# Kernel optimization log

Measured on AMD Instinct MI355X. Metric: run time of the kernel, lower is better.

Reference implementation:

```python
import jax, jax.numpy as jnp
import numpy as np

EMB = 1024
HEADS = 8
SEQ = 4096
LN_EPS = 1e-5


def _layernorm(x, g, b):
    mu = jnp.mean(x, axis=-1, keepdims=True)
    var = jnp.mean(jnp.square(x - mu), axis=-1, keepdims=True)
    return (x - mu) * jax.lax.rsqrt(var + LN_EPS) * g + b


def setup_inputs() -> dict:
    key = jax.random.key(0)
    ks = jax.random.split(key, 12)
    s = 1.0 / np.sqrt(EMB)
    sz = 1.0 / np.sqrt(EMB * HEADS)
    return {
        "history": jax.random.normal(ks[0], (SEQ, EMB), jnp.float32),
        "embdding": jax.random.normal(ks[1], (SEQ, EMB), jnp.float32),
        # per-head Linear weights, torch layout [out, in], stacked over heads
        "Wq_w": jax.random.uniform(ks[2], (HEADS, EMB, EMB), jnp.float32, -s, s),
        "Wq_b": jax.random.uniform(ks[3], (HEADS, EMB), jnp.float32, -s, s),
        "Wk_w": jax.random.uniform(ks[4], (HEADS, EMB, EMB), jnp.float32, -s, s),
        "Wk_b": jax.random.uniform(ks[5], (HEADS, EMB), jnp.float32, -s, s),
        "Wv_w": jax.random.uniform(ks[6], (HEADS, EMB, EMB), jnp.float32, -s, s),
        "Wv_b": jax.random.uniform(ks[7], (HEADS, EMB), jnp.float32, -s, s),
        "Wz_w": jax.random.uniform(ks[8], (EMB, EMB * HEADS), jnp.float32, -sz, sz),
        "Wz_b": jax.random.uniform(ks[9], (EMB,), jnp.float32, -sz, sz),
        "ln1_g": jnp.ones((EMB,), jnp.float32),
        "ln1_b": jnp.zeros((EMB,), jnp.float32),
        "Wf_w": jax.random.uniform(ks[10], (EMB, EMB), jnp.float32, -s, s),
        "Wf_b": jax.random.uniform(ks[11], (EMB,), jnp.float32, -s, s),
        "ln2_g": jnp.ones((EMB,), jnp.float32),
        "ln2_b": jnp.zeros((EMB,), jnp.float32),
    }


def reference(history, embdding, Wq_w, Wq_b, Wk_w, Wk_b, Wv_w, Wv_b,
              Wz_w, Wz_b, ln1_g, ln1_b, Wf_w, Wf_b, ln2_g, ln2_b):
    S, E = embdding.shape
    H = Wq_w.shape[0]
    # per-head linears (torch: y = x @ W.T + b), batched over heads
    Q = jnp.einsum('se,hfe->hsf', embdding, Wq_w) + Wq_b[:, None, :]  # [H,S,E]
    K = jnp.einsum('se,hfe->hsf', embdding, Wk_w) + Wk_b[:, None, :]
    V = jnp.einsum('se,hfe->hsf', history, Wv_w) + Wv_b[:, None, :]
    # K^T @ Q -> [H, E, E], softmax over dim=1 of the 2D matrix == last axis here
    scores = jnp.einsum('hse,hsf->hef', K, Q) / jnp.sqrt(jnp.asarray(E, Q.dtype))
    A = jax.nn.softmax(scores, axis=-1)  # [H,E,E]
    Zh = jnp.einsum('hse,hef->hsf', V, A)  # [H,S,E]
    Z = jnp.transpose(Zh, (1, 0, 2)).reshape(S, H * E)  # cat(dim=1) in head order
    O = Z @ Wz_w.T + Wz_b  # [S,E]
    LN1 = _layernorm(O, ln1_g, ln1_b) + embdding
    FN = LN1 @ Wf_w.T + Wf_b
    LN2 = _layernorm(FN, ln2_g, ln2_b) + LN1
    return LN2
```

## Files before the change

### kernel.cpp

```cpp
#include <hip/hip_runtime.h>


constexpr int EMB = 1024;
constexpr int SEQ = 4096;
constexpr int NH  = 8;

using f32x4  = __attribute__((ext_vector_type(4))) float;
using bf16x8 = __attribute__((ext_vector_type(8))) __bf16;
using us8    = __attribute__((ext_vector_type(8))) unsigned short;

#define GLOAD_LDS16(g, l) __builtin_amdgcn_global_load_lds(                 \
    (const __attribute__((address_space(1))) void*)(g),                     \
    (__attribute__((address_space(3))) void*)(l), 16, 0, 0)

__device__ inline unsigned short f2bf(float x) {
  unsigned int u = __float_as_uint(x);
  u += 0x7FFFu + ((u >> 16) & 1u);
  return (unsigned short)(u >> 16);
}
__device__ inline float bf2f(unsigned short h) {
  return __uint_as_float(((unsigned int)h) << 16);
}

constexpr int NB_DOTB = 4096;
constexpr int NB_ROWB = 1664;
constexpr int NB_XT   = 1024;

__global__ __launch_bounds__(256) void mega_cvt_k(
    const float* __restrict__ Wk, const float* __restrict__ Wq,
    const float* __restrict__ hist, const float* __restrict__ Wz,
    const float* __restrict__ Wf, const float* __restrict__ emb,
    const float* __restrict__ Wv, const float* __restrict__ xbar,
    unsigned short* __restrict__ Wkb, unsigned short* __restrict__ Wqb,
    unsigned short* __restrict__ Yb, unsigned short* __restrict__ Wzb,
    unsigned short* __restrict__ Wfb, unsigned short* __restrict__ XT,
    unsigned short* __restrict__ WvT,
    float* __restrict__ u, float* __restrict__ v) {
  __shared__ float tileT[64][65];
  const int b = blockIdx.x, tid = threadIdx.x;

  if (b < NB_DOTB) {
    int gw = b * 4 + (tid >> 6);
    int lane = tid & 63;
    const float* src = (gw < 8192) ? Wk : Wq;
    unsigned short* dst = (gw < 8192) ? Wkb : Wqb;
    float* dot = (gw < 8192) ? u : v;
    int row = gw & 8191;
    const float4* sr = (const float4*)(src + (size_t)row * EMB);
    const float4* xb4 = (const float4*)xbar;
    ushort4* d4 = (ushort4*)(dst + (size_t)row * EMB);
    float s = 0.f;
#pragma unroll
    for (int j = 0; j < 4; ++j) {
      int idx = j * 64 + lane;
      float4 x = sr[idx];
      float4 xb = xb4[idx];
      ushort4 o; o.x = f2bf(x.x); o.y = f2bf(x.y); o.z = f2bf(x.z); o.w = f2bf(x.w);
      d4[idx] = o;
      s += x.x * xb.x + x.y * xb.y + x.z * xb.z + x.w * xb.w;
    }
#pragma unroll
    for (int off = 32; off; off >>= 1) s += __shfl_down(s, off);
    if (lane == 0) dot[row] = s;
  } else if (b < NB_DOTB + NB_ROWB) {
    size_t f0 = (size_t)(b - NB_DOTB) * 8192;
    const float* src; unsigned short* dst; size_t loc;
    if (f0 < 4194304ull) { src = hist; dst = Yb; loc = f0; }
    else if (f0 < 12582912ull) { src = Wz; dst = Wzb; loc = f0 - 4194304ull; }
    else { src = Wf; dst = Wfb; loc = f0 - 12582912ull; }
#pragma unroll
    for (int p = 0; p < 8; ++p) {
      int i = p * 256 + tid;
      float4 x = ((const float4*)(src + loc))[i];
      ushort4 o; o.x = f2bf(x.x); o.y = f2bf(x.y); o.z = f2bf(x.z); o.w = f2bf(x.w);
      ((ushort4*)(dst + loc))[i] = o;
    }
  } else {
    int tb = b - (NB_DOTB + NB_ROWB);
    const float* src; unsigned short* dst; int R, r0, c0;
    if (tb < NB_XT) {
      src = emb; dst = XT; R = SEQ;
      r0 = (tb >> 4) * 64; c0 = (tb & 15) * 64;
    } else {
      int t2 = tb - NB_XT, z = t2 >> 8, tt = t2 & 255;
      src = Wv + (size_t)z * EMB * EMB; dst = WvT + (size_t)z * EMB * EMB;
      R = EMB;
      r0 = (tt >> 4) * 64; c0 = (tt & 15) * 64;
    }
    int tx = tid & 15, ty = tid >> 4;
#pragma unroll
    for (int p = 0; p < 4; ++p) {
      int ir = p * 16 + ty;
      float4 x = *(const float4*)(src + (size_t)(r0 + ir) * EMB + c0 + tx * 4);
      tileT[tx * 4 + 0][ir] = x.x; tileT[tx * 4 + 1][ir] = x.y;
      tileT[tx * 4 + 2][ir] = x.z; tileT[tx * 4 + 3][ir] = x.w;
    }
    __syncthreads();
#pragma unroll
    for (int p = 0; p < 4; ++p) {
      int orow = p * 16 + ty;
      ushort4 o;
      o.x = f2bf(tileT[orow][tx * 4 + 0]);
      o.y = f2bf(tileT[orow][tx * 4 + 1]);
      o.z = f2bf(tileT[orow][tx * 4 + 2]);
      o.w = f2bf(tileT[orow][tx * 4 + 3]);
      *(ushort4*)(dst + (size_t)(c0 + orow) * R + r0 + tx * 4) = o;
    }
  }
}

__global__ __launch_bounds__(256) void colsum_part_k(const float* __restrict__ X,
                                                     float* __restrict__ part) {
  int e = blockIdx.x * 256 + threadIdx.x;
  int y = blockIdx.y;
  float s = 0.f;
  for (int r = y * 128; r < y * 128 + 128; ++r) s += X[(size_t)r * EMB + e];
  part[y * EMB + e] = s;
}
__global__ __launch_bounds__(256) void colsum_red_k(const float* __restrict__ part,
                                                    float* __restrict__ xbar) {
  int e = blockIdx.x * 256 + threadIdx.x;
  float s = 0.f;
  for (int y = 0; y < 32; ++y) s += part[y * EMB + e];
  xbar[e] = s;
}

__global__ __launch_bounds__(256) void dvec_k(const unsigned short* __restrict__ Wzb,
                                              const float* __restrict__ bz,
                                              const float* __restrict__ c,
                                              float* __restrict__ d) {
  __shared__ float sb[4];
  int g = blockIdx.x, tid = threadIdx.x;
  const unsigned short* row = Wzb + (size_t)g * (NH * EMB);
  float s = 0.f;
#pragma unroll
  for (int p = 0; p < 4; ++p) {
    int i = p * 256 + tid;
    us8 w = ((const us8*)row)[i];
    float4 c0 = ((const float4*)c)[i * 2];
    float4 c1 = ((const float4*)c)[i * 2 + 1];
    s += bf2f(w[0]) * c0.x + bf2f(w[1]) * c0.y + bf2f(w[2]) * c0.z + bf2f(w[3]) * c0.w;
    s += bf2f(w[4]) * c1.x + bf2f(w[5]) * c1.y + bf2f(w[6]) * c1.z + bf2f(w[7]) * c1.w;
  }
  int lane = tid & 63, w = tid >> 6;
#pragma unroll
  for (int off = 32; off; off >>= 1) s += __shfl_down(s, off);
  if (lane == 0) sb[w] = s;
  __syncthreads();
  if (tid == 0) d[g] = bz[g] + sb[0] + sb[1] + sb[2] + sb[3];
}

__global__ __launch_bounds__(256) void mred_tr_k(const unsigned short* __restrict__ Mp,
                                                 unsigned short* __restrict__ MT) {
  __shared__ float t[32][33];
  int g0 = blockIdx.x * 32, e0 = blockIdx.y * 32;
  int tx = threadIdx.x & 31, ty = threadIdx.x >> 5;
#pragma unroll
  for (int k = 0; k < 4; ++k) {
    int e = e0 + ty + k * 8;
    float s = 0.f;
#pragma unroll
    for (int h = 0; h < NH; ++h)
      s += bf2f(Mp[((size_t)h << 20) + (size_t)e * EMB + g0 + tx]);
    t[ty + k * 8][tx] = s;
  }
  __syncthreads();
#pragma unroll
  for (int k = 0; k < 4; ++k) {
    int r = ty + k * 8;
    MT[(size_t)(g0 + r) * EMB + e0 + tx] = f2bf(t[tx][r]);
  }
}

__global__ __launch_bounds__(256) void gram_red_k(const unsigned short* __restrict__ Gp,
                                                  unsigned short* __restrict__ Gbf) {
  int i = blockIdx.x * 256 + threadIdx.x;
  float4 s = {0.f, 0.f, 0.f, 0.f};
#pragma unroll
  for (int z = 0; z < 8; ++z) {
    ushort4 v = ((const ushort4*)(Gp + (size_t)z * EMB * EMB))[i];
    s.x += bf2f(v.x); s.y += bf2f(v.y); s.z += bf2f(v.z); s.w += bf2f(v.w);
  }
  ushort4 o; o.x = f2bf(s.x); o.y = f2bf(s.y); o.z = f2bf(s.z); o.w = f2bf(s.w);
  ((ushort4*)Gbf)[i] = o;
}

__global__ __launch_bounds__(256) void colstat1_k(const unsigned short* __restrict__ ScT,
                                                  float* __restrict__ m_part,
                                                  float* __restrict__ s_part) {
  int col = blockIdx.x * 256 + threadIdx.x;
  int rc = blockIdx.y, h = blockIdx.z;
  const unsigned short* base = ScT + ((size_t)h * EMB + rc * 64) * EMB + col;
  float m = -1e30f, s = 0.f;
#pragma unroll 4
  for (int r = 0; r < 64; ++r) {
    float x = bf2f(base[(size_t)r * EMB]);
    float nm = fmaxf(m, x);
    s = s * __expf(m - nm) + __expf(x - nm);
    m = nm;
  }
  m_part[((size_t)h * 16 + rc) * EMB + col] = m;
  s_part[((size_t)h * 16 + rc) * EMB + col] = s;
}

__global__ __launch_bounds__(256) void colstat2_k(const float* __restrict__ m_part,
                                                  const float* __restrict__ s_part,
                                                  float* __restrict__ mfin,
                                                  float* __restrict__ isfin) {
  int i = blockIdx.x * 256 + threadIdx.x;
  int h = i >> 10, col = i & 1023;
  float M = -1e30f, S = 0.f;
#pragma unroll
  for (int c = 0; c < 16; ++c) {
    float m = m_part[((size_t)h * 16 + c) * EMB + col];
    float s = s_part[((size_t)h * 16 + c) * EMB + col];
    float nm = fmaxf(M, m);
    S = S * __expf(M - nm) + s * __expf(m - nm);
    M = nm;
  }
  mfin[i] = M;
  isfin[i] = 1.0f / S;
}

__global__ __launch_bounds__(256) void at_cvec_k(const unsigned short* __restrict__ ScT,
                                                 const float* __restrict__ mfin,
                                                 const float* __restrict__ isfin,
                                                 const float* __restrict__ bv,
                                                 unsigned short* __restrict__ AT,
                                                 float* __restrict__ cbuf) {
  __shared__ float sb[4];
  int f = blockIdx.x, h = blockIdx.y, tid = threadIdx.x;
  size_t rowoff = ((size_t)h * EMB + f) * EMB;
  ushort4 xr = ((const ushort4*)(ScT + rowoff))[tid];
  float4 m  = ((const float4*)(mfin + (size_t)h * EMB))[tid];
  float4 is = ((const float4*)(isfin + (size_t)h * EMB))[tid];
  float4 b  = ((const float4*)(bv + (size_t)h * EMB))[tid];
  float a0 = __expf(bf2f(xr.x) - m.x) * is.x;
  float a1 = __expf(bf2f(xr.y) - m.y) * is.y;
  float a2 = __expf(bf2f(xr.z) - m.z) * is.z;
  float a3 = __expf(bf2f(xr.w) - m.w) * is.w;
  ushort4 o; o.x = f2bf(a0); o.y = f2bf(a1); o.z = f2bf(a2); o.w = f2bf(a3);
  ((ushort4*)(AT + rowoff))[tid] = o;
  float s = a0 * b.x + a1 * b.y + a2 * b.z + a3 * b.w;
  int lane = tid & 63, w = tid >> 6;
#pragma unroll
  for (int off = 32; off; off >>= 1) s += __shfl_down(s, off);
  if (lane == 0) sb[w] = s;
  __syncthreads();
  if (tid == 0) cbuf[h * EMB + f] = sb[0] + sb[1] + sb[2] + sb[3];
}

__global__ __launch_bounds__(256) void layernorm_k(const float* __restrict__ Xin,
                                                   const float* __restrict__ resid,
                                                   const float* __restrict__ gw,
                                                   const float* __restrict__ bw,
                                                   float* __restrict__ outf,
                                                   unsigned short* __restrict__ outb) {
  __shared__ float sb[16];
  int row = blockIdx.x, tid = threadIdx.x;
  float4 v = ((const float4*)(Xin + (size_t)row * EMB))[tid];
  float s = v.x + v.y + v.z + v.w;
  float q = v.x * v.x + v.y * v.y + v.z * v.z + v.w * v.w;
  int lane = tid & 63, w = tid >> 6;
#pragma unroll
  for (int off = 32; off; off >>= 1) { s += __shfl_down(s, off); q += __shfl_down(q, off); }
  if (lane == 0) { sb[w] = s; sb[8 + w] = q; }
  __syncthreads();
  float mu  = (sb[0] + sb[1] + sb[2] + sb[3]) * (1.0f / EMB);
  float var = (sb[8] + sb[9] + sb[10] + sb[11]) * (1.0f / EMB) - mu * mu;
  float rs = rsqrtf(var + 1e-5f);
  float4 rv = ((const float4*)(resid + (size_t)row * EMB))[tid];
  float4 gv = ((const float4*)gw)[tid];
  float4 bv = ((const float4*)bw)[tid];
  float o0 = (v.x - mu) * rs * gv.x + bv.x + rv.x;
  float o1 = (v.y - mu) * rs * gv.y + bv.y + rv.y;
  float o2 = (v.z - mu) * rs * gv.z + bv.z + rv.z;
  float o3 = (v.w - mu) * rs * gv.w + bv.w + rv.w;
  float4 ov; ov.x = o0; ov.y = o1; ov.z = o2; ov.w = o3;
  ((float4*)(outf + (size_t)row * EMB))[tid] = ov;
  if (outb) {
    ushort4 ob; ob.x = f2bf(o0); ob.y = f2bf(o1); ob.z = f2bf(o2); ob.w = f2bf(o3);
    ((ushort4*)(outb + (size_t)row * EMB))[tid] = ob;
  }
}

template <int MODE>
__global__ __launch_bounds__(256) void gemm_nt(const unsigned short* __restrict__ A,
                                               const unsigned short* __restrict__ B,
                                               void* __restrict__ Cout,
                                               int K, int lda, int ldb, int ldc,
                                               long long aZ, long long bZ, long long cZ,
                                               int nx, int ny,
                                               const float* __restrict__ e0,
                                               const float* __restrict__ e1,
                                               const float* __restrict__ e2,
                                               const float* __restrict__ e3) {
  const int q = gridDim.x >> 3;
  const int wg = (blockIdx.x & 7) * q + (blockIdx.x >> 3);
  const int bx = wg % nx;
  const int by = (wg / nx) % ny;
  const int z  = wg / (nx * ny);
  A += (size_t)z * aZ;
  B += (size_t)z * bZ;
  const int tid = threadIdx.x;
  const int lane = tid & 63, wid = tid >> 6;
  const int wm = wid >> 1, wn = wid & 1;
  const int row0 = bx * 64, col0 = by * 128;

  __shared__ __align__(16) unsigned short lds[(64 + 128) * 64];
  unsigned short* As = lds;
  unsigned short* Bs = lds + 64 * 64;

  f32x4 acc[2][4] = {};
  const int lrow = lane & 15, kg = lane >> 4;
  const int lr = lane >> 3;
  const int lc = (lane & 7) * 8;

  const int nt = K >> 6;
  for (int t = 0; t < nt; ++t) {
    const int k0 = t << 6;
#pragma unroll
    for (int c = 0; c < 2; ++c) {
      int chunk = wid * 2 + c;
      int r = chunk * 8 + lr;
      GLOAD_LDS16(A + (size_t)(row0 + r) * lda + k0 + lc, &As[chunk * 512]);
    }
#pragma unroll
    for (int c = 0; c < 4; ++c) {
      int chunk = wid * 4 + c;
      int r = chunk * 8 + lr;
      GLOAD_LDS16(B + (size_t)(col0 + r) * ldb + k0 + lc, &Bs[chunk * 512]);
    }
    __syncthreads();
#pragma unroll
    for (int ks = 0; ks < 2; ++ks) {
      bf16x8 a[2], b[4];
      int koff = ks * 32 + kg * 8;
#pragma unroll
      for (int i = 0; i < 2; ++i)
        a[i] = *(const bf16x8*)&As[(wm * 32 + i * 16 + lrow) * 64 + koff];
#pragma unroll
      for (int j = 0; j < 4; ++j)
        b[j] = *(const bf16x8*)&Bs[(wn * 64 + j * 16 + lrow) * 64 + koff];
#pragma unroll
      for (int i = 0; i < 2; ++i)
#pragma unroll
        for (int j = 0; j < 4; ++j)
          acc[i][j] = __builtin_amdgcn_mfma_f32_16x16x32_bf16(a[i], b[j], acc[i][j], 0, 0, 0);
    }
    __syncthreads();
  }

  const int rb = (lane >> 4) * 4, cc = lane & 15;
  if (MODE == 1 || MODE == 4) {
    unsigned short* Cs = lds;
#pragma unroll
    for (int i = 0; i < 2; ++i) {
#pragma unroll
      for (int j = 0; j < 4; ++j) {
#pragma unroll
        for (int r = 0; r < 4; ++r) {
          float val = acc[i][j][r];
          int mm = wm * 32 + i * 16 + rb + r;
          int nn = wn * 64 + j * 16 + cc;
          if (MODE == 4) {
            int m = row0 + mm, n = col0 + nn;
            float bq = e0[z * EMB + m], uu = e1[z * EMB + n];
            float bk = e2[z * EMB + n], vv = e3[z * EMB + m];
            val = (val + bq * (uu + (float)SEQ * bk) + vv * bk) * (1.0f / 32.0f);
          }
          Cs[mm * 128 + nn] = f2bf(val);
        }
      }
    }
    __syncthreads();
    unsigned short* Cg = (unsigned short*)Cout + (size_t)z * cZ;
#pragma unroll
    for (int p = 0; p < 4; ++p) {
      int idx = p * 256 + tid;
      int row = idx >> 4, col = (idx & 15) * 8;
      *(us8*)(Cg + (size_t)(row0 + row) * ldc + col0 + col) =
          *(const us8*)&Cs[row * 128 + col];
    }
  } else {
#pragma unroll
    for (int i = 0; i < 2; ++i) {
#pragma unroll
      for (int j = 0; j < 4; ++j) {
#pragma unroll
        for (int r = 0; r < 4; ++r) {
          int m = row0 + wm * 32 + i * 16 + rb + r;
          int n = col0 + wn * 64 + j * 16 + cc;
          size_t off = (size_t)z * cZ + (size_t)m * ldc + n;
          ((float*)Cout)[off] = acc[i][j][r] + e0[n];
        }
      }
    }
  }
}

extern "C" void kernel_launch(void* const* d_in, const int* in_sizes, int n_in,
                              void* d_out, int out_size, void* d_ws, size_t ws_size,
                              hipStream_t stream) {
  const float* history = (const float*)d_in[0];
  const float* emb     = (const float*)d_in[1];
  const float* Wq_w = (const float*)d_in[2];
  const float* Wq_b = (const float*)d_in[3];
  const float* Wk_w = (const float*)d_in[4];
  const float* Wk_b = (const float*)d_in[5];
  const float* Wv_w = (const float*)d_in[6];
  const float* Wv_b = (const float*)d_in[7];
  const float* Wz_w = (const float*)d_in[8];
  const float* Wz_b = (const float*)d_in[9];
  const float* ln1_g = (const float*)d_in[10];
  const float* ln1_b = (const float*)d_in[11];
  const float* Wf_w = (const float*)d_in[12];
  const float* Wf_b = (const float*)d_in[13];
  const float* ln2_g = (const float*)d_in[14];
  const float* ln2_b = (const float*)d_in[15];

  char* ws = (char*)d_ws;
  const size_t MB = 1024ull * 1024ull;
  unsigned short* XT  = (unsigned short*)(ws + 0);
  unsigned short* Ybf = (unsigned short*)(ws + 8 * MB);
  unsigned short* Wkb = (unsigned short*)(ws + 16 * MB);
  unsigned short* Wqb = (unsigned short*)(ws + 32 * MB);
  unsigned short* WvT = (unsigned short*)(ws + 48 * MB);
  unsigned short* Wzb = (unsigned short*)(ws + 64 * MB);
  unsigned short* Wfb = (unsigned short*)(ws + 80 * MB);
  unsigned short* Gbf = (unsigned short*)(ws + 82 * MB);
  float* xpart = (float*)(ws + 84 * MB);
  float* xbar  = (float*)(ws + 84 * MB + 160 * 1024);
  float* ubuf  = (float*)(ws + 84 * MB + 192 * 1024);
  float* vbuf  = (float*)(ws + 84 * MB + 256 * 1024);
  float* cbuf  = (float*)(ws + 84 * MB + 320 * 1024);
  float* dbuf  = (float*)(ws + 84 * MB + 384 * 1024);
  unsigned short* Tbf = (unsigned short*)(ws + 85 * MB);
  float* Sc  = (float*)(ws + 101 * MB);
  char*  St  = ws + 133 * MB;
  unsigned short* ATb = (unsigned short*)(ws + 149 * MB);
  unsigned short* MTb = (unsigned short*)(ws + 165 * MB);
  float* m_part = (float*)(St);
  float* s_part = (float*)(St + 512 * 1024);
  float* mfin   = (float*)(St + 1024 * 1024);
  float* isfin  = (float*)(St + 1056 * 1024);
  unsigned short* Gp  = (unsigned short*)Sc;
  unsigned short* ScT = (unsigned short*)Sc;
  unsigned short* Cbf = Tbf;
  unsigned short* Mp  = (unsigned short*)Sc;
  float* Obuf = (float*)St;
  float* LN1  = (float*)ATb;
  unsigned short* LN1b = XT;
  float* FN   = (float*)Tbf;
  const long long EE = (long long)EMB * EMB;

  colsum_part_k<<<dim3(4, 32), 256, 0, stream>>>(emb, xpart);
  colsum_red_k<<<dim3(4), 256, 0, stream>>>(xpart, xbar);

  mega_cvt_k<<<dim3(8832), 256, 0, stream>>>(Wk_w, Wq_w, history, Wz_w, Wf_w,
                                             emb, Wv_w, xbar,
                                             Wkb, Wqb, Ybf, Wzb, Wfb, XT, WvT,
                                             ubuf, vbuf);

  gemm_nt<1><<<dim3(1024), 256, 0, stream>>>(XT, XT, Gp, 512, SEQ, SEQ, EMB,
                                             512, 512, EE, 16, 8,
                                             nullptr, nullptr, nullptr, nullptr);
  gram_red_k<<<dim3(EMB * EMB / 4 / 256), 256, 0, stream>>>(Gp, Gbf);
  gemm_nt<1><<<dim3(1024), 256, 0, stream>>>(Wqb, Gbf, Tbf, EMB, EMB, EMB, EMB,
                                             EE, 0, EE, 16, 8,
                                             nullptr, nullptr, nullptr, nullptr);
  gemm_nt<4><<<dim3(1024), 256, 0, stream>>>(Tbf, Wkb, ScT, EMB, EMB, EMB, EMB,
                                             EE, EE, EE, 16, 8,
                                             Wq_b, ubuf, Wk_b, vbuf);
  colstat1_k<<<dim3(4, 16, NH), 256, 0, stream>>>(ScT, m_part, s_part);
  colstat2_k<<<dim3(32), 256, 0, stream>>>(m_part, s_part, mfin, isfin);
  at_cvec_k<<<dim3(EMB, NH), 256, 0, stream>>>(ScT, mfin, isfin, Wv_b, ATb, cbuf);
  gemm_nt<1><<<dim3(1024), 256, 0, stream>>>(WvT, ATb, Cbf, EMB, EMB, EMB, EMB,
                                             EE, EE, EE, 16, 8,
                                             nullptr, nullptr, nullptr, nullptr);
  gemm_nt<1><<<dim3(1024), 256, 0, stream>>>(Cbf, Wzb, Mp, EMB, EMB, NH * EMB, EMB,
                                             EE, (long long)EMB, EE, 16, 8,
                                             nullptr, nullptr, nullptr, nullptr);
  mred_tr_k<<<dim3(EMB / 32, EMB / 32), 256, 0, stream>>>(Mp, MTb);
  dvec_k<<<dim3(EMB), 256, 0, stream>>>(Wzb, Wz_b, cbuf, dbuf);
  gemm_nt<3><<<dim3(512), 256, 0, stream>>>(Ybf, MTb, Obuf, EMB, EMB, EMB, EMB,
                                            0, 0, 0, 64, 8,
                                            dbuf, nullptr, nullptr, nullptr);
  layernorm_k<<<dim3(SEQ), 256, 0, stream>>>(Obuf, emb, ln1_g, ln1_b, LN1, LN1b);
  gemm_nt<3><<<dim3(512), 256, 0, stream>>>(LN1b, Wfb, FN, EMB, EMB, EMB, EMB,
                                            0, 0, 0, 64, 8,
                                            Wf_b, nullptr, nullptr, nullptr);
  layernorm_k<<<dim3(SEQ), 256, 0, stream>>>(FN, LN1, ln2_g, ln2_b, (float*)d_out, nullptr);
}
```

Before: 292.6 us.

## Co-schedule independent kernels: fold Gram GEMM into conversion kernel and dvec into Mp GEMM

Moves the emb transpose/bf16 conversion into the column-sum kernel, then launches the Gram GEMM in the same grid as the weight conversions so the two independent jobs run concurrently. The dvec reduction likewise shares a launch with the Mp GEMM. The GEMM body becomes a shared device function. This removes launches and tail idle time, at the cost of heterogeneous blocks competing for memory bandwidth and LDS.

```diff
diff --git a/kernel.cpp b/kernel.cpp
--- a/kernel.cpp
+++ b/kernel.cpp
@@ -22,31 +22,204 @@
   return __uint_as_float(((unsigned int)h) << 16);
 }
 
-constexpr int NB_DOTB = 4096;
-constexpr int NB_ROWB = 1664;
-constexpr int NB_XT   = 1024;
-
-__global__ __launch_bounds__(256) void mega_cvt_k(
+template <int MODE>
+__device__ __attribute__((always_inline)) void gemm_body(
+    unsigned short* lds, int wg,
+    const unsigned short* A, const unsigned short* B, void* Cout,
+    int K, int lda, int ldb, int ldc,
+    long long aZ, long long bZ, long long cZ, int nx, int ny,
+    const float* e0, const float* e1, const float* e2, const float* e3) {
+  const int bx = wg % nx;
+  const int by = (wg / nx) % ny;
+  const int z  = wg / (nx * ny);
+  A += (size_t)z * aZ;
+  B += (size_t)z * bZ;
+  const int tid = threadIdx.x;
+  const int lane = tid & 63, wid = tid >> 6;
+  const int wm = wid >> 1, wn = wid & 1;
+  const int row0 = bx * 64, col0 = by * 128;
+
+  unsigned short* As = lds;
+  unsigned short* Bs = lds + 64 * 64;
+
+  f32x4 acc[2][4] = {};
+  const int lrow = lane & 15, kg = lane >> 4;
+  const int lr = lane >> 3;
+  const int lc = (lane & 7) * 8;
+
+  const int nt = K >> 6;
+  for (int t = 0; t < nt; ++t) {
+    const int k0 = t << 6;
+#pragma unroll
+    for (int c = 0; c < 2; ++c) {
+      int chunk = wid * 2 + c;
+      int r = chunk * 8 + lr;
+      GLOAD_LDS16(A + (size_t)(row0 + r) * lda + k0 + lc, &As[chunk * 512]);
+    }
+#pragma unroll
+    for (int c = 0; c < 4; ++c) {
+      int chunk = wid * 4 + c;
+      int r = chunk * 8 + lr;
+      GLOAD_LDS16(B + (size_t)(col0 + r) * ldb + k0 + lc, &Bs[chunk * 512]);
+    }
+    __syncthreads();
+#pragma unroll
+    for (int ks = 0; ks < 2; ++ks) {
+      bf16x8 a[2], b[4];
+      int koff = ks * 32 + kg * 8;
+#pragma unroll
+      for (int i = 0; i < 2; ++i)
+        a[i] = *(const bf16x8*)&As[(wm * 32 + i * 16 + lrow) * 64 + koff];
+#pragma unroll
+      for (int j = 0; j < 4; ++j)
+        b[j] = *(const bf16x8*)&Bs[(wn * 64 + j * 16 + lrow) * 64 + koff];
+#pragma unroll
+      for (int i = 0; i < 2; ++i)
+#pragma unroll
+        for (int j = 0; j < 4; ++j)
+          acc[i][j] = __builtin_amdgcn_mfma_f32_16x16x32_bf16(a[i], b[j], acc[i][j], 0, 0, 0);
+    }
+    __syncthreads();
+  }
+
+  const int rb = (lane >> 4) * 4, cc = lane & 15;
+  if (MODE == 1 || MODE == 4) {
+    unsigned short* Cs = lds;
+#pragma unroll
+    for (int i = 0; i < 2; ++i) {
+#pragma unroll
+      for (int j = 0; j < 4; ++j) {
+#pragma unroll
+        for (int r = 0; r < 4; ++r) {
+          float val = acc[i][j][r];
+          int mm = wm * 32 + i * 16 + rb + r;
+          int nn = wn * 64 + j * 16 + cc;
+          if (MODE == 4) {
+            int m = row0 + mm, n = col0 + nn;
+            float bq = e0[z * EMB + m], uu = e1[z * EMB + n];
+            float bk = e2[z * EMB + n], vv = e3[z * EMB + m];
+            val = (val + bq * (uu + (float)SEQ * bk) + vv * bk) * (1.0f / 32.0f);
+          }
+          Cs[mm * 128 + nn] = f2bf(val);
+        }
+      }
+    }
+    __syncthreads();
+    unsigned short* Cg = (unsigned short*)Cout + (size_t)z * cZ;
+#pragma unroll
+    for (int p = 0; p < 4; ++p) {
+      int idx = p * 256 + tid;
+      int row = idx >> 4, col = (idx & 15) * 8;
+      *(us8*)(Cg + (size_t)(row0 + row) * ldc + col0 + col) =
+          *(const us8*)&Cs[row * 128 + col];
+    }
+  } else {
+#pragma unroll
+    for (int i = 0; i < 2; ++i) {
+#pragma unroll
+      for (int j = 0; j < 4; ++j) {
+#pragma unroll
+        for (int r = 0; r < 4; ++r) {
+          int m = row0 + wm * 32 + i * 16 + rb + r;
+          int n = col0 + wn * 64 + j * 16 + cc;
+          size_t off = (size_t)z * cZ + (size_t)m * ldc + n;
+          ((float*)Cout)[off] = acc[i][j][r] + e0[n];
+        }
+      }
+    }
+  }
+}
+
+template <int MODE>
+__global__ __launch_bounds__(256) void gemm_nt(const unsigned short* __restrict__ A,
+                                               const unsigned short* __restrict__ B,
+                                               void* __restrict__ Cout,
+                                               int K, int lda, int ldb, int ldc,
+                                               long long aZ, long long bZ, long long cZ,
+                                               int nx, int ny,
+                                               const float* __restrict__ e0,
+                                               const float* __restrict__ e1,
+                                               const float* __restrict__ e2,
+                                               const float* __restrict__ e3) {
+  __shared__ __align__(16) unsigned short lds[(64 + 128) * 64];
+  const int q = gridDim.x >> 3;
+  const int wg = (blockIdx.x & 7) * q + (blockIdx.x >> 3);
+  gemm_body<MODE>(lds, wg, A, B, Cout, K, lda, ldb, ldc, aZ, bZ, cZ, nx, ny,
+                  e0, e1, e2, e3);
+}
+
+__global__ __launch_bounds__(256) void colsum_xt_k(const float* __restrict__ emb,
+                                                   float* __restrict__ part,
+                                                   unsigned short* __restrict__ XT) {
+  __shared__ float tileT[64][65];
+  const int b = blockIdx.x, tid = threadIdx.x;
+  if (b < 128) {
+    int e = (b & 3) * 256 + tid;
+    int y = b >> 2;
+    float s = 0.f;
+    for (int r = y * 128; r < y * 128 + 128; ++r) s += emb[(size_t)r * EMB + e];
+    part[y * EMB + e] = s;
+    return;
+  }
+  int tb = b - 128;
+  int r0 = (tb >> 4) * 64, c0 = (tb & 15) * 64;
+  int tx = tid & 15, ty = tid >> 4;
+#pragma unroll
+  for (int p = 0; p < 4; ++p) {
+    int ir = p * 16 + ty;
+    float4 x = *(const float4*)(emb + (size_t)(r0 + ir) * EMB + c0 + tx * 4);
+    tileT[tx * 4 + 0][ir] = x.x; tileT[tx * 4 + 1][ir] = x.y;
+    tileT[tx * 4 + 2][ir] = x.z; tileT[tx * 4 + 3][ir] = x.w;
+  }
+  __syncthreads();
+#pragma unroll
+  for (int p = 0; p < 4; ++p) {
+    int orow = p * 16 + ty;
+    ushort4 o;
+    o.x = f2bf(tileT[orow][tx * 4 + 0]);
+    o.y = f2bf(tileT[orow][tx * 4 + 1]);
+    o.z = f2bf(tileT[orow][tx * 4 + 2]);
+    o.w = f2bf(tileT[orow][tx * 4 + 3]);
+    *(ushort4*)(XT + (size_t)(c0 + orow) * SEQ + r0 + tx * 4) = o;
+  }
+}
+
+__global__ __launch_bounds__(256) void colsum_red_k(const float* __restrict__ part,
+                                                    float* __restrict__ xbar) {
+  int e = blockIdx.x * 256 + threadIdx.x;
+  float s = 0.f;
+  for (int y = 0; y < 32; ++y) s += part[y * EMB + e];
+  xbar[e] = s;
+}
+
+__global__ __launch_bounds__(256) void gram_cvt_k(
+    const unsigned short* __restrict__ XT, unsigned short* __restrict__ Gp,
     const float* __restrict__ Wk, const float* __restrict__ Wq,
     const float* __restrict__ hist, const float* __restrict__ Wz,
-    const float* __restrict__ Wf, const float* __restrict__ emb,
-    const float* __restrict__ Wv, const float* __restrict__ xbar,
+    const float* __restrict__ Wf, const float* __restrict__ Wv,
+    const float* __restrict__ xbar,
     unsigned short* __restrict__ Wkb, unsigned short* __restrict__ Wqb,
     unsigned short* __restrict__ Yb, unsigned short* __restrict__ Wzb,
-    unsigned short* __restrict__ Wfb, unsigned short* __restrict__ XT,
-    unsigned short* __restrict__ WvT,
+    unsigned short* __restrict__ Wfb, unsigned short* __restrict__ WvT,
     float* __restrict__ u, float* __restrict__ v) {
-  __shared__ float tileT[64][65];
-  const int b = blockIdx.x, tid = threadIdx.x;
-
-  if (b < NB_DOTB) {
-    int gw = b * 4 + (tid >> 6);
+  __shared__ __align__(16) unsigned short smem[(64 + 128) * 64];
+  const int tid = threadIdx.x;
+  if (blockIdx.x < 1024) {
+    const int wg = ((int)blockIdx.x & 7) * 128 + ((int)blockIdx.x >> 3);
+    gemm_body<1>(smem, wg, XT, XT, Gp, 512, SEQ, SEQ, EMB,
+                 512, 512, (long long)EMB * EMB, 16, 8,
+                 nullptr, nullptr, nullptr, nullptr);
+    return;
+  }
+  int b2 = blockIdx.x - 1024;
+  if (b2 < 4096) {
+    int gw = b2 * 4 + (tid >> 6);
     int lane = tid & 63;
     const float* src = (gw < 8192) ? Wk : Wq;
     unsigned short* dst = (gw < 8192) ? Wkb : Wqb;
     float* dot = (gw < 8192) ? u : v;
     int row = gw & 8191;
-    const float4* sr = (const float4*)(src + (size_t)row * EMB);
+    const float4* sr  = (const float4*)(src + (size_t)row * EMB);
     const float4* xb4 = (const float4*)xbar;
     ushort4* d4 = (ushort4*)(dst + (size_t)row * EMB);
     float s = 0.f;
@@ -62,8 +235,8 @@
 #pragma unroll
     for (int off = 32; off; off >>= 1) s += __shfl_down(s, off);
     if (lane == 0) dot[row] = s;
-  } else if (b < NB_DOTB + NB_ROWB) {
-    size_t f0 = (size_t)(b - NB_DOTB) * 8192;
+  } else if (b2 < 5760) {
+    size_t f0 = (size_t)(b2 - 4096) * 8192;
     const float* src; unsigned short* dst; size_t loc;
     if (f0 < 4194304ull) { src = hist; dst = Yb; loc = f0; }
     else if (f0 < 12582912ull) { src = Wz; dst = Wzb; loc = f0 - 4194304ull; }
@@ -76,17 +249,11 @@
       ((ushort4*)(dst + loc))[i] = o;
     }
   } else {
-    int tb = b - (NB_DOTB + NB_ROWB);
-    const float* src; unsigned short* dst; int R, r0, c0;
-    if (tb < NB_XT) {
-      src = emb; dst = XT; R = SEQ;
-      r0 = (tb >> 4) * 64; c0 = (tb & 15) * 64;
-    } else {
-      int t2 = tb - NB_XT, z = t2 >> 8, tt = t2 & 255;
-      src = Wv + (size_t)z * EMB * EMB; dst = WvT + (size_t)z * EMB * EMB;
-      R = EMB;
-      r0 = (tt >> 4) * 64; c0 = (tt & 15) * 64;
-    }
+    int t2 = b2 - 5760, z = t2 >> 8, tt = t2 & 255;
+    const float* src = Wv + (size_t)z * EMB * EMB;
+    unsigned short* dst = WvT + (size_t)z * EMB * EMB;
+    int r0 = (tt >> 4) * 64, c0 = (tt & 15) * 64;
+    float (*tileT)[65] = (float(*)[65])smem;
     int tx = tid & 15, ty = tid >> 4;
 #pragma unroll
     for (int p = 0; p < 4; ++p) {
@@ -104,41 +271,35 @@
       o.y = f2bf(tileT[orow][tx * 4 + 1]);
       o.z = f2bf(tileT[orow][tx * 4 + 2]);
       o.w = f2bf(tileT[orow][tx * 4 + 3]);
-      *(ushort4*)(dst + (size_t)(c0 + orow) * R + r0 + tx * 4) = o;
-    }
-  }
-}
-
-__global__ __launch_bounds__(256) void colsum_part_k(const float* __restrict__ X,
-                                                     float* __restrict__ part) {
-  int e = blockIdx.x * 256 + threadIdx.x;
-  int y = blockIdx.y;
-  float s = 0.f;
-  for (int r = y * 128; r < y * 128 + 128; ++r) s += X[(size_t)r * EMB + e];
-  part[y * EMB + e] = s;
-}
-__global__ __launch_bounds__(256) void colsum_red_k(const float* __restrict__ part,
-                                                    float* __restrict__ xbar) {
-  int e = blockIdx.x * 256 + threadIdx.x;
-  float s = 0.f;
-  for (int y = 0; y < 32; ++y) s += part[y * EMB + e];
-  xbar[e] = s;
-}
-
-__global__ __launch_bounds__(256) void dvec_k(const unsigned short* __restrict__ Wzb,
-                                              const float* __restrict__ bz,
-                                              const float* __restrict__ c,
-                                              float* __restrict__ d) {
-  __shared__ float sb[4];
-  int g = blockIdx.x, tid = threadIdx.x;
+      *(ushort4*)(dst + (size_t)(c0 + orow) * EMB + r0 + tx * 4) = o;
+    }
+  }
+}
+
+__global__ __launch_bounds__(256) void mp_dvec_k(
+    const unsigned short* __restrict__ Cbf, const unsigned short* __restrict__ Wzb,
+    unsigned short* __restrict__ Mp,
+    const float* __restrict__ bz, const float* __restrict__ cvec,
+    float* __restrict__ d) {
+  __shared__ __align__(16) unsigned short smem[(64 + 128) * 64];
+  const int tid = threadIdx.x;
+  if (blockIdx.x < 1024) {
+    const int wg = ((int)blockIdx.x & 7) * 128 + ((int)blockIdx.x >> 3);
+    gemm_body<1>(smem, wg, Cbf, Wzb, Mp, EMB, EMB, NH * EMB, EMB,
+                 (long long)EMB * EMB, (long long)EMB, (long long)EMB * EMB, 16, 8,
+                 nullptr, nullptr, nullptr, nullptr);
+    return;
+  }
+  int g = blockIdx.x - 1024;
+  float* sb = (float*)smem;
   const unsigned short* row = Wzb + (size_t)g * (NH * EMB);
   float s = 0.f;
 #pragma unroll
   for (int p = 0; p < 4; ++p) {
     int i = p * 256 + tid;
     us8 w = ((const us8*)row)[i];
-    float4 c0 = ((const float4*)c)[i * 2];
-    float4 c1 = ((const float4*)c)[i * 2 + 1];
+    float4 c0 = ((const float4*)cvec)[i * 2];
+    float4 c1 = ((const float4*)cvec)[i * 2 + 1];
     s += bf2f(w[0]) * c0.x + bf2f(w[1]) * c0.y + bf2f(w[2]) * c0.z + bf2f(w[3]) * c0.w;
     s += bf2f(w[4]) * c1.x + bf2f(w[5]) * c1.y + bf2f(w[6]) * c1.z + bf2f(w[7]) * c1.w;
   }
@@ -281,121 +442,6 @@
   if (outb) {
     ushort4 ob; ob.x = f2bf(o0); ob.y = f2bf(o1); ob.z = f2bf(o2); ob.w = f2bf(o3);
     ((ushort4*)(outb + (size_t)row * EMB))[tid] = ob;
-  }
-}
-
-template <int MODE>
-__global__ __launch_bounds__(256) void gemm_nt(const unsigned short* __restrict__ A,
-                                               const unsigned short* __restrict__ B,
-                                               void* __restrict__ Cout,
-                                               int K, int lda, int ldb, int ldc,
-                                               long long aZ, long long bZ, long long cZ,
-                                               int nx, int ny,
-                                               const float* __restrict__ e0,
-                                               const float* __restrict__ e1,
-                                               const float* __restrict__ e2,
-                                               const float* __restrict__ e3) {
-  const int q = gridDim.x >> 3;
-  const int wg = (blockIdx.x & 7) * q + (blockIdx.x >> 3);
-  const int bx = wg % nx;
-  const int by = (wg / nx) % ny;
-  const int z  = wg / (nx * ny);
-  A += (size_t)z * aZ;
-  B += (size_t)z * bZ;
-  const int tid = threadIdx.x;
-  const int lane = tid & 63, wid = tid >> 6;
-  const int wm = wid >> 1, wn = wid & 1;
-  const int row0 = bx * 64, col0 = by * 128;
-
-  __shared__ __align__(16) unsigned short lds[(64 + 128) * 64];
-  unsigned short* As = lds;
-  unsigned short* Bs = lds + 64 * 64;
-
-  f32x4 acc[2][4] = {};
-  const int lrow = lane & 15, kg = lane >> 4;
-  const int lr = lane >> 3;
-  const int lc = (lane & 7) * 8;
-
-  const int nt = K >> 6;
-  for (int t = 0; t < nt; ++t) {
-    const int k0 = t << 6;
-#pragma unroll
-    for (int c = 0; c < 2; ++c) {
-      int chunk = wid * 2 + c;
-      int r = chunk * 8 + lr;
-      GLOAD_LDS16(A + (size_t)(row0 + r) * lda + k0 + lc, &As[chunk * 512]);
-    }
-#pragma unroll
-    for (int c = 0; c < 4; ++c) {
-      int chunk = wid * 4 + c;
-      int r = chunk * 8 + lr;
-      GLOAD_LDS16(B + (size_t)(col0 + r) * ldb + k0 + lc, &Bs[chunk * 512]);
-    }
-    __syncthreads();
-#pragma unroll
-    for (int ks = 0; ks < 2; ++ks) {
-      bf16x8 a[2], b[4];
-      int koff = ks * 32 + kg * 8;
-#pragma unroll
-      for (int i = 0; i < 2; ++i)
-        a[i] = *(const bf16x8*)&As[(wm * 32 + i * 16 + lrow) * 64 + koff];
-#pragma unroll
-      for (int j = 0; j < 4; ++j)
-        b[j] = *(const bf16x8*)&Bs[(wn * 64 + j * 16 + lrow) * 64 + koff];
-#pragma unroll
-      for (int i = 0; i < 2; ++i)
-#pragma unroll
-        for (int j = 0; j < 4; ++j)
-          acc[i][j] = __builtin_amdgcn_mfma_f32_16x16x32_bf16(a[i], b[j], acc[i][j], 0, 0, 0);
-    }
-    __syncthreads();
-  }
-
-  const int rb = (lane >> 4) * 4, cc = lane & 15;
-  if (MODE == 1 || MODE == 4) {
-    unsigned short* Cs = lds;
-#pragma unroll
-    for (int i = 0; i < 2; ++i) {
-#pragma unroll
-      for (int j = 0; j < 4; ++j) {
-#pragma unroll
-        for (int r = 0; r < 4; ++r) {
-          float val = acc[i][j][r];
-          int mm = wm * 32 + i * 16 + rb + r;
-          int nn = wn * 64 + j * 16 + cc;
-          if (MODE == 4) {
-            int m = row0 + mm, n = col0 + nn;
-            float bq = e0[z * EMB + m], uu = e1[z * EMB + n];
-            float bk = e2[z * EMB + n], vv = e3[z * EMB + m];
-            val = (val + bq * (uu + (float)SEQ * bk) + vv * bk) * (1.0f / 32.0f);
-          }
-          Cs[mm * 128 + nn] = f2bf(val);
-        }
-      }
-    }
-    __syncthreads();
-    unsigned short* Cg = (unsigned short*)Cout + (size_t)z * cZ;
-#pragma unroll
-    for (int p = 0; p < 4; ++p) {
-      int idx = p * 256 + tid;
-      int row = idx >> 4, col = (idx & 15) * 8;
-      *(us8*)(Cg + (size_t)(row0 + row) * ldc + col0 + col) =
-          *(const us8*)&Cs[row * 128 + col];
-    }
-  } else {
-#pragma unroll
-    for (int i = 0; i < 2; ++i) {
-#pragma unroll
-      for (int j = 0; j < 4; ++j) {
-#pragma unroll
-        for (int r = 0; r < 4; ++r) {
-          int m = row0 + wm * 32 + i * 16 + rb + r;
-          int n = col0 + wn * 64 + j * 16 + cc;
-          size_t off = (size_t)z * cZ + (size_t)m * ldc + n;
-          ((float*)Cout)[off] = acc[i][j][r] + e0[n];
-        }
-      }
-    }
   }
 }
 
@@ -454,17 +500,14 @@
   float* FN   = (float*)Tbf;
   const long long EE = (long long)EMB * EMB;
 
-  colsum_part_k<<<dim3(4, 32), 256, 0, stream>>>(emb, xpart);
+  colsum_xt_k<<<dim3(1152), 256, 0, stream>>>(emb, xpart, XT);
   colsum_red_k<<<dim3(4), 256, 0, stream>>>(xpart, xbar);
 
-  mega_cvt_k<<<dim3(8832), 256, 0, stream>>>(Wk_w, Wq_w, history, Wz_w, Wf_w,
-                                             emb, Wv_w, xbar,
-                                             Wkb, Wqb, Ybf, Wzb, Wfb, XT, WvT,
+  gram_cvt_k<<<dim3(8832), 256, 0, stream>>>(XT, Gp,
+                                             Wk_w, Wq_w, history, Wz_w, Wf_w, Wv_w,
+                                             xbar,
+                                             Wkb, Wqb, Ybf, Wzb, Wfb, WvT,
                                              ubuf, vbuf);
-
-  gemm_nt<1><<<dim3(1024), 256, 0, stream>>>(XT, XT, Gp, 512, SEQ, SEQ, EMB,
-                                             512, 512, EE, 16, 8,
-                                             nullptr, nullptr, nullptr, nullptr);
   gram_red_k<<<dim3(EMB * EMB / 4 / 256), 256, 0, stream>>>(Gp, Gbf);
   gemm_nt<1><<<dim3(1024), 256, 0, stream>>>(Wqb, Gbf, Tbf, EMB, EMB, EMB, EMB,
                                              EE, 0, EE, 16, 8,
@@ -478,11 +521,8 @@
   gemm_nt<1><<<dim3(1024), 256, 0, stream>>>(WvT, ATb, Cbf, EMB, EMB, EMB, EMB,
                                              EE, EE, EE, 16, 8,
                                              nullptr, nullptr, nullptr, nullptr);
-  gemm_nt<1><<<dim3(1024), 256, 0, stream>>>(Cbf, Wzb, Mp, EMB, EMB, NH * EMB, EMB,
-                                             EE, (long long)EMB, EE, 16, 8,
-                                             nullptr, nullptr, nullptr, nullptr);
+  mp_dvec_k<<<dim3(2048), 256, 0, stream>>>(Cbf, Wzb, Mp, Wz_b, cbuf, dbuf);
   mred_tr_k<<<dim3(EMB / 32, EMB / 32), 256, 0, stream>>>(Mp, MTb);
-  dvec_k<<<dim3(EMB), 256, 0, stream>>>(Wzb, Wz_b, cbuf, dbuf);
   gemm_nt<3><<<dim3(512), 256, 0, stream>>>(Ybf, MTb, Obuf, EMB, EMB, EMB, EMB,
                                             0, 0, 0, 64, 8,
                                             dbuf, nullptr, nullptr, nullptr);
```

Result: faster. 282.4 us (-3.5%).
